# Optimization experiments

Measured on AMD Instinct MI355X. Metric: run time of the kernel, lower is better.

## Reference

```python
import jax, jax.numpy as jnp
import numpy as np
from jax import lax

STRIDES = (8, 16, 32)
FEAT_SIZES = ((80, 80), (40, 40), (20, 20))  # 640x640 input
NUM_CLASSES = 80
NMS_THR = 0.65
SCORE_THR = 0.01
NMS_PRE = 1000
MAX_PER_IMG = 100


def make_points():
    # MlvlPointGenerator.grid_priors with offset=0, with_stride=True.
    pts = []
    for (h, w), s in zip(FEAT_SIZES, STRIDES):
        y, x = jnp.meshgrid(jnp.arange(h, dtype=jnp.float32),
                            jnp.arange(w, dtype=jnp.float32), indexing='ij')
        pts.append(jnp.stack([x.ravel() * s, y.ravel() * s,
                              jnp.full(h * w, float(s)),
                              jnp.full(h * w, float(s))], axis=-1))
    return jnp.concatenate(pts, axis=0)  # [P, 4] = (px, py, sx, sy)


def decode_boxes(points, reg):
    # YOLOXBBoxDecoder: xy = reg[:2]*stride + point; wh = exp(reg[2:])*stride
    xys = reg[..., :2] * points[..., 2:] + points[..., :2]
    whs = jnp.exp(reg[..., 2:]) * points[..., 2:]
    half = whs * 0.5
    return jnp.concatenate([xys - half, xys + half], axis=-1)  # [..., 4] xyxy


def pairwise_iou(b):
    # b: [N, 4] xyxy
    area = (b[:, 2] - b[:, 0]) * (b[:, 3] - b[:, 1])
    lt = jnp.maximum(b[:, None, :2], b[None, :, :2])
    rb = jnp.minimum(b[:, None, 2:], b[None, :, 2:])
    wh = jnp.clip(rb - lt, 0.0)
    inter = wh[..., 0] * wh[..., 1]
    return inter / (area[:, None] + area[None, :] - inter + 1e-9)


def nms_image(cls_s, boxes, obj):
    # cls_s: [P, C] sigmoid scores, boxes: [P, 4], obj: [P] sigmoid objectness
    max_scores = jnp.max(cls_s, axis=-1)
    labels = jnp.argmax(cls_s, axis=-1)
    scores = max_scores * obj
    masked = jnp.where(scores >= SCORE_THR, scores, -1.0)
    top_scores, top_idx = lax.top_k(masked, NMS_PRE)  # sorted descending
    valid = top_scores >= SCORE_THR
    b = boxes[top_idx]            # [K, 4]
    lab = labels[top_idx]         # [K]
    # batched_nms: offset boxes per class so cross-class boxes never overlap
    off = lab.astype(b.dtype)[:, None] * (jnp.max(jnp.abs(b)) + 1.0)
    iou = pairwise_iou(b + off)   # [K, K]
    idx = jnp.arange(NMS_PRE)

    def body(i, keep):
        sup = (iou[i] > NMS_THR) & keep[i] & (idx > i)
        return keep & ~sup

    keep = lax.fori_loop(0, NMS_PRE, body, valid)
    # compact kept detections (score-sorted order preserved), pad to MAX_PER_IMG
    order = jnp.argsort(~keep, stable=True)[:MAX_PER_IMG]
    k = keep[order]
    out_b = jnp.where(k[:, None], b[order], 0.0)
    out_s = jnp.where(k, top_scores[order], 0.0)
    out_l = jnp.where(k, lab[order], -1)
    return out_b, out_s, out_l


def setup_inputs() -> dict:
    key = jax.random.key(0)
    ks = jax.random.split(key, 9)
    shapes = {
        'cls0': (32, NUM_CLASSES, 80, 80), 'cls1': (32, NUM_CLASSES, 40, 40),
        'cls2': (32, NUM_CLASSES, 20, 20),
        'reg0': (32, 4, 80, 80), 'reg1': (32, 4, 40, 40), 'reg2': (32, 4, 20, 20),
        'obj0': (32, 1, 80, 80), 'obj1': (32, 1, 40, 40), 'obj2': (32, 1, 20, 20),
    }
    return {n: jax.random.normal(k, s, dtype=jnp.float32)
            for (n, s), k in zip(shapes.items(), ks)}


def reference(cls0, cls1, cls2, reg0, reg1, reg2, obj0, obj1, obj2):
    def flat(xs, c):
        return jnp.concatenate(
            [jnp.transpose(x, (0, 2, 3, 1)).reshape(x.shape[0], -1, c) for x in xs],
            axis=1)
    cls = flat([cls0, cls1, cls2], NUM_CLASSES)   # [N, P, C]
    reg = flat([reg0, reg1, reg2], 4)             # [N, P, 4]
    obj = flat([obj0, obj1, obj2], 1)[..., 0]     # [N, P]
    points = make_points()                        # [P, 4]
    boxes = decode_boxes(points[None], reg)       # [N, P, 4]
    cls = jax.nn.sigmoid(cls)
    obj = jax.nn.sigmoid(obj)
    return jax.vmap(nms_image)(cls, boxes, obj)   # ([N,M,4],[N,M],[N,M] labels)
```

## Files before the change

### kernel.cpp

```cpp
#include <hip/hip_runtime.h>
#include <stdint.h>

#define N_IMG 32
#define P_TOT 8400
#define NCLS 80
#define NMS_PRE 1000
#define MAXOUT 100
#define SCORE_THRF 0.01f
#define NMS_THRF 0.65f
#define CAND_N 2048
#define NB 512
#define BINBASE 8192
#define TIE_EPS 0.05f


__device__ __forceinline__ float sigmoidf_(float x) { return 1.0f / (1.0f + expf(-x)); }

__global__ __launch_bounds__(256) void k_score(
    const float* __restrict__ cls0, const float* __restrict__ cls1, const float* __restrict__ cls2,
    const float* __restrict__ obj0, const float* __restrict__ obj1, const float* __restrict__ obj2,
    uint64_t* __restrict__ keys)
{
    __shared__ float    pml[4][64];
    __shared__ uint64_t part[4][64];
    int lane = threadIdx.x & 63, wid = threadIdx.x >> 6;
    int a = blockIdx.x * 64 + lane;
    int n = a / P_TOT;
    int p = a - n * P_TOT;

    const float* cl; const float* ob; int HW, q;
    if (p < 6400)      { cl = cls0; ob = obj0; HW = 6400; q = p; }
    else if (p < 8000) { cl = cls1; ob = obj1; HW = 1600; q = p - 6400; }
    else               { cl = cls2; ob = obj2; HW = 400;  q = p - 8000; }

    const float* cbase = cl + (size_t)n * NCLS * HW + q;
    int c0 = wid * 20;

    float lg[20];
    #pragma unroll
    for (int i = 0; i < 20; ++i)
        lg[i] = cbase[(size_t)(c0 + i) * HW];
    __builtin_amdgcn_sched_group_barrier(0x20, 20, 0);

    float a0 = fmaxf(lg[0], lg[1]),  a1 = fmaxf(lg[2], lg[3]);
    float a2 = fmaxf(lg[4], lg[5]),  a3 = fmaxf(lg[6], lg[7]);
    float a4 = fmaxf(lg[8], lg[9]),  a5 = fmaxf(lg[10], lg[11]);
    float a6 = fmaxf(lg[12], lg[13]), a7 = fmaxf(lg[14], lg[15]);
    float a8 = fmaxf(lg[16], lg[17]), a9 = fmaxf(lg[18], lg[19]);
    float b0 = fmaxf(a0, a1), b1 = fmaxf(a2, a3), b2 = fmaxf(a4, a5);
    float b3 = fmaxf(a6, a7), b4 = fmaxf(a8, a9);
    float lmax = fmaxf(fmaxf(fmaxf(b0, b1), fmaxf(b2, b3)), b4);
    pml[wid][lane] = lmax;
    __syncthreads();

    float gmaxl = fmaxf(fmaxf(pml[0][lane], pml[1][lane]),
                        fmaxf(pml[2][lane], pml[3][lane]));
    float thr = gmaxl - TIE_EPS;
    uint64_t m = 0;
    #pragma unroll
    for (int i = 0; i < 20; ++i) {
        if (lg[i] >= thr) {
            float s = sigmoidf_(lg[i]);
            uint64_t pk = ((uint64_t)__float_as_uint(s) << 8) | (uint32_t)(79 - (c0 + i));
            m = m > pk ? m : pk;
        }
    }
    part[wid][lane] = m;
    __syncthreads();

    if (wid == 0) {
        uint64_t m0 = part[0][lane], m1 = part[1][lane];
        uint64_t m2 = part[2][lane], m3 = part[3][lane];
        uint64_t ma = m0 > m1 ? m0 : m1, mb = m2 > m3 ? m2 : m3;
        uint64_t mm = ma > mb ? ma : mb;
        float best = __uint_as_float((uint32_t)(mm >> 8));
        int bc = 79 - (int)(mm & 0xFFu);

        float so = sigmoidf_(ob[(size_t)n * HW + q]);
        float sc = __fmul_rn(best, so);
        float masked = (sc >= SCORE_THRF) ? sc : -1.0f;
        uint32_t u = __float_as_uint(masked);
        uint32_t ord = (u & 0x80000000u) ? ~u : (u | 0x80000000u);
        uint32_t dk = ~ord;
        keys[a] = ((uint64_t)dk << 32) | (uint32_t)((p << 8) | bc);
    }
}

__global__ __launch_bounds__(1024) void k_selnms(
    const uint64_t* __restrict__ keys,
    const float* __restrict__ reg0, const float* __restrict__ reg1, const float* __restrict__ reg2,
    float* __restrict__ out)
{
    __shared__ __align__(16) char big[60416];
    __shared__ int   s_misc[2];
    __shared__ float fsh[17];
    __shared__ int   kidx[MAXOUT];

    uint64_t* cand    = (uint64_t*)big;
    uint32_t* hist    = (uint32_t*)(big + 16384);
    uint32_t* base    = (uint32_t*)(big + 18432);
    uint32_t* fill    = (uint32_t*)(big + 20480);
    uint64_t* grouped = (uint64_t*)(big + 22528);
    float4* s_obx = (float4*)(big + 16384);
    float*  s_oar = (float*) (big + 32384);
    float4* s_raw = (float4*)(big + 36384);
    float2* s_sl  = (float2*)(big + 52384);

    int n = blockIdx.x, tid = threadIdx.x;

    if (tid < NB) { hist[tid] = 0; fill[tid] = 0; }
    for (int t = tid; t < CAND_N; t += 1024) cand[t] = ~0ull;
    __syncthreads();

    #pragma unroll
    for (int it = 0; it < 9; ++it) {
        int t = tid + it * 1024;
        if (t < P_TOT) {
            uint64_t k = keys[(size_t)n * P_TOT + t];
            uint32_t dk = (uint32_t)(k >> 32);
            if (!(dk & 0x80000000u)) atomicAdd(&hist[(dk >> 17) - BINBASE], 1u);
        }
    }
    __syncthreads();

    if (tid < 64) {
        uint32_t c[8]; uint32_t s = 0;
        #pragma unroll
        for (int i = 0; i < 8; ++i) { c[i] = hist[tid * 8 + i]; s += c[i]; }
        uint32_t inc = s;
        #pragma unroll
        for (int o = 1; o < 64; o <<= 1) {
            uint32_t v = __shfl_up(inc, o);
            if (tid >= o) inc += v;
        }
        uint32_t excl = inc - s;
        uint32_t b = excl;
        #pragma unroll
        for (int i = 0; i < 8; ++i) { base[tid * 8 + i] = b; b += c[i]; }
        uint32_t total = __shfl(inc, 63);
        uint32_t target = total < (uint32_t)NMS_PRE ? total : (uint32_t)NMS_PRE;
        uint32_t cum = excl; int found = 0x7fffffff;
        #pragma unroll
        for (int i = 0; i < 8; ++i) {
            cum += c[i];
            if (found == 0x7fffffff && cum >= target && target > 0) found = tid * 8 + i;
        }
        #pragma unroll
        for (int o = 32; o > 0; o >>= 1) { int f = __shfl_xor(found, o); found = f < found ? f : found; }
        if (tid == 0) { s_misc[0] = (total > 0) ? found : -1; s_misc[1] = (int)target; }
    }
    __syncthreads();
    int Bcut = s_misc[0];

    #pragma unroll
    for (int it = 0; it < 9; ++it) {
        int t = tid + it * 1024;
        if (t < P_TOT) {
            uint64_t k = keys[(size_t)n * P_TOT + t];
            uint32_t dk = (uint32_t)(k >> 32);
            if (!(dk & 0x80000000u)) {
                int bin = (int)((dk >> 17) - BINBASE);
                if (bin <= Bcut) {
                    uint32_t pos = base[bin] + atomicAdd(&fill[bin], 1u);
                    if (pos < CAND_N) grouped[pos] = k;
                }
            }
        }
    }
    __syncthreads();

    int ccnt = 0;
    if (Bcut >= 0) {
        uint32_t cc = base[Bcut] + hist[Bcut];
        ccnt = cc < (uint32_t)CAND_N ? (int)cc : CAND_N;
    }
    for (int s = tid; s < ccnt; s += 1024) {
        uint64_t k = grouped[s];
        uint32_t dk = (uint32_t)(k >> 32);
        int bin = (int)((dk >> 17) - BINBASE);
        uint32_t b0 = base[bin];
        uint32_t e0 = b0 + hist[bin]; if (e0 > (uint32_t)CAND_N) e0 = CAND_N;
        uint32_t r = b0;
        for (uint32_t t = b0; t < e0; ++t) r += (grouped[t] < k) ? 1u : 0u;
        if (r < (uint32_t)CAND_N) cand[r] = k;
    }
    int V = s_misc[1];
    __syncthreads();

    float4 bx = make_float4(0.f, 0.f, 0.f, 0.f);
    float scm = -1.0f, labf = 0.f, m = 0.f;
    if (tid < NMS_PRE) {
        uint64_t key = cand[tid];
        uint32_t dk = (uint32_t)(key >> 32);
        if (!(dk & 0x80000000u)) {
            uint32_t low = (uint32_t)key;
            int lab = (int)(low & 0xFFu);
            int p   = (int)(low >> 8);
            uint32_t ord = ~dk;
            scm = __uint_as_float(ord ^ 0x80000000u);

            const float* rg; int HW, q, W; float s;
            if (p < 6400)      { rg = reg0; HW = 6400; q = p;        W = 80; s = 8.f; }
            else if (p < 8000) { rg = reg1; HW = 1600; q = p - 6400; W = 40; s = 16.f; }
            else               { rg = reg2; HW = 400;  q = p - 8000; W = 20; s = 32.f; }

            float px = (float)(q % W) * s;
            float py = (float)(q / W) * s;
            const float* rb = rg + (size_t)n * 4 * HW + q;
            float dx = rb[0], dy = rb[HW], dw = rb[2 * HW], dh = rb[3 * HW];
            float cx = __fadd_rn(__fmul_rn(dx, s), px);
            float cy = __fadd_rn(__fmul_rn(dy, s), py);
            float hw = __fmul_rn(__fmul_rn(expf(dw), s), 0.5f);
            float hh = __fmul_rn(__fmul_rn(expf(dh), s), 0.5f);
            bx.x = __fsub_rn(cx, hw); bx.y = __fsub_rn(cy, hh);
            bx.z = __fadd_rn(cx, hw); bx.w = __fadd_rn(cy, hh);
            labf = (float)lab;
            m = fmaxf(fmaxf(fabsf(bx.x), fabsf(bx.y)), fmaxf(fabsf(bx.z), fabsf(bx.w)));
        }
    }

    #pragma unroll
    for (int o = 32; o > 0; o >>= 1) m = fmaxf(m, __shfl_xor(m, o));
    if ((tid & 63) == 0) fsh[tid >> 6] = m;
    __syncthreads();
    if (tid == 0) {
        float g = fsh[0];
        #pragma unroll
        for (int w = 1; w < 16; ++w) g = fmaxf(g, fsh[w]);
        fsh[16] = g;
    }
    __syncthreads();
    float gmax = fsh[16];

    if (tid < NMS_PRE) {
        float off = __fmul_rn(labf, __fadd_rn(gmax, 1.0f));
        float x1 = __fadd_rn(bx.x, off), y1 = __fadd_rn(bx.y, off);
        float x2 = __fadd_rn(bx.z, off), y2 = __fadd_rn(bx.w, off);
        s_obx[tid] = make_float4(x1, y1, x2, y2);
        s_oar[tid] = __fmul_rn(__fsub_rn(x2, x1), __fsub_rn(y2, y1));
        s_raw[tid] = bx;
        s_sl[tid]  = make_float2(scm, labf);
    }
    __syncthreads();
    if (tid >= 64) return;

    int lane = tid;
    int count = 0;
    float k1x1 = 0.f, k1y1 = 0.f, k1x2 = 0.f, k1y2 = 0.f, k1a = 0.f;
    float k2x1 = 0.f, k2y1 = 0.f, k2x2 = 0.f, k2y2 = 0.f, k2a = 0.f;

    float4 nb = s_obx[0]; float na = s_oar[0];
    for (int i = 0; i < V && count < MAXOUT; ++i) {
        float4 cb = nb; float ca = na;
        int ip = (i + 1 < V) ? i + 1 : i;
        nb = s_obx[ip]; na = s_oar[ip];

        bool sup = false;
        int c1 = count < 64 ? count : 64;
        if (lane < c1) {
            float ltx = fmaxf(k1x1, cb.x), lty = fmaxf(k1y1, cb.y);
            float rbx = fminf(k1x2, cb.z), rby = fminf(k1y2, cb.w);
            float w = fmaxf(__fsub_rn(rbx, ltx), 0.f);
            float h = fmaxf(__fsub_rn(rby, lty), 0.f);
            float inter = __fmul_rn(w, h);
            float denom = __fadd_rn(__fsub_rn(__fadd_rn(k1a, ca), inter), 1e-9f);
            sup = (inter / denom > NMS_THRF);
        }
        if (count > 64 && lane < count - 64) {
            float ltx = fmaxf(k2x1, cb.x), lty = fmaxf(k2y1, cb.y);
            float rbx = fminf(k2x2, cb.z), rby = fminf(k2y2, cb.w);
            float w = fmaxf(__fsub_rn(rbx, ltx), 0.f);
            float h = fmaxf(__fsub_rn(rby, lty), 0.f);
            float inter = __fmul_rn(w, h);
            float denom = __fadd_rn(__fsub_rn(__fadd_rn(k2a, ca), inter), 1e-9f);
            sup = sup || (inter / denom > NMS_THRF);
        }
        if (__ballot(sup) == 0ull) {
            if (lane == count)      { k1x1 = cb.x; k1y1 = cb.y; k1x2 = cb.z; k1y2 = cb.w; k1a = ca; }
            if (lane + 64 == count) { k2x1 = cb.x; k2y1 = cb.y; k2x2 = cb.z; k2y2 = cb.w; k2a = ca; }
            if (lane == 0) kidx[count] = i;
            ++count;
        }
    }

    float* ob = out;
    float* os = out + N_IMG * MAXOUT * 4;
    float* ol = os + N_IMG * MAXOUT;
    for (int mi = lane; mi < MAXOUT; mi += 64) {
        int o4 = (n * MAXOUT + mi) * 4;
        if (mi < count) {
            int i = kidx[mi];
            float4 b  = s_raw[i];
            float2 sl = s_sl[i];
            ob[o4 + 0] = b.x; ob[o4 + 1] = b.y; ob[o4 + 2] = b.z; ob[o4 + 3] = b.w;
            os[n * MAXOUT + mi] = sl.x;
            ol[n * MAXOUT + mi] = sl.y;
        } else {
            ob[o4 + 0] = 0.f; ob[o4 + 1] = 0.f; ob[o4 + 2] = 0.f; ob[o4 + 3] = 0.f;
            os[n * MAXOUT + mi] = 0.f;
            ol[n * MAXOUT + mi] = -1.f;
        }
    }
}

extern "C" void kernel_launch(void* const* d_in, const int* in_sizes, int n_in,
                              void* d_out, int out_size, void* d_ws, size_t ws_size,
                              hipStream_t stream)
{
    const float* cls0 = (const float*)d_in[0];
    const float* cls1 = (const float*)d_in[1];
    const float* cls2 = (const float*)d_in[2];
    const float* reg0 = (const float*)d_in[3];
    const float* reg1 = (const float*)d_in[4];
    const float* reg2 = (const float*)d_in[5];
    const float* obj0 = (const float*)d_in[6];
    const float* obj1 = (const float*)d_in[7];
    const float* obj2 = (const float*)d_in[8];

    uint64_t* keys = (uint64_t*)d_ws;
    float* out = (float*)d_out;

    k_score<<<(N_IMG * P_TOT) / 64, 256, 0, stream>>>(
        cls0, cls1, cls2, obj0, obj1, obj2, keys);
    k_selnms<<<N_IMG, 1024, 0, stream>>>(keys, reg0, reg1, reg2, out);
}
```

Measured before the change: 67.85 us.

## Process all classes per thread in score kernel; cache bin ids in LDS

```diff
diff --git a/kernel.cpp b/kernel.cpp
--- a/kernel.cpp
+++ b/kernel.cpp
@@ -21,10 +21,8 @@
     const float* __restrict__ obj0, const float* __restrict__ obj1, const float* __restrict__ obj2,
     uint64_t* __restrict__ keys)
 {
-    __shared__ float    pml[4][64];
-    __shared__ uint64_t part[4][64];
-    int lane = threadIdx.x & 63, wid = threadIdx.x >> 6;
-    int a = blockIdx.x * 64 + lane;
+    int wid = threadIdx.x >> 6, lane = threadIdx.x & 63;
+    int a = (blockIdx.x * 4 + wid) * 64 + lane;
     int n = a / P_TOT;
     int p = a - n * P_TOT;
 
@@ -34,56 +32,51 @@
     else               { cl = cls2; ob = obj2; HW = 400;  q = p - 8000; }
 
     const float* cbase = cl + (size_t)n * NCLS * HW + q;
-    int c0 = wid * 20;
-
-    float lg[20];
-    #pragma unroll
-    for (int i = 0; i < 20; ++i)
-        lg[i] = cbase[(size_t)(c0 + i) * HW];
-    __builtin_amdgcn_sched_group_barrier(0x20, 20, 0);
-
-    float a0 = fmaxf(lg[0], lg[1]),  a1 = fmaxf(lg[2], lg[3]);
-    float a2 = fmaxf(lg[4], lg[5]),  a3 = fmaxf(lg[6], lg[7]);
-    float a4 = fmaxf(lg[8], lg[9]),  a5 = fmaxf(lg[10], lg[11]);
-    float a6 = fmaxf(lg[12], lg[13]), a7 = fmaxf(lg[14], lg[15]);
-    float a8 = fmaxf(lg[16], lg[17]), a9 = fmaxf(lg[18], lg[19]);
-    float b0 = fmaxf(a0, a1), b1 = fmaxf(a2, a3), b2 = fmaxf(a4, a5);
-    float b3 = fmaxf(a6, a7), b4 = fmaxf(a8, a9);
-    float lmax = fmaxf(fmaxf(fmaxf(b0, b1), fmaxf(b2, b3)), b4);
-    pml[wid][lane] = lmax;
-    __syncthreads();
-
-    float gmaxl = fmaxf(fmaxf(pml[0][lane], pml[1][lane]),
-                        fmaxf(pml[2][lane], pml[3][lane]));
+
+    float objv = ob[(size_t)n * HW + q];
+    float lg[NCLS];
+    #pragma unroll
+    for (int i = 0; i < NCLS; ++i)
+        lg[i] = cbase[(size_t)i * HW];
+    __builtin_amdgcn_sched_group_barrier(0x20, 81, 0);
+    #pragma unroll
+    for (int i = 0; i < NCLS; ++i)
+        asm volatile("" : "+v"(lg[i]));
+
+    float t40[40];
+    #pragma unroll
+    for (int i = 0; i < 40; ++i) t40[i] = fmaxf(lg[2 * i], lg[2 * i + 1]);
+    float t20[20];
+    #pragma unroll
+    for (int i = 0; i < 20; ++i) t20[i] = fmaxf(t40[2 * i], t40[2 * i + 1]);
+    float t10[10];
+    #pragma unroll
+    for (int i = 0; i < 10; ++i) t10[i] = fmaxf(t20[2 * i], t20[2 * i + 1]);
+    float t5[5];
+    #pragma unroll
+    for (int i = 0; i < 5; ++i) t5[i] = fmaxf(t10[2 * i], t10[2 * i + 1]);
+    float gmaxl = fmaxf(fmaxf(fmaxf(t5[0], t5[1]), fmaxf(t5[2], t5[3])), t5[4]);
+
     float thr = gmaxl - TIE_EPS;
     uint64_t m = 0;
     #pragma unroll
-    for (int i = 0; i < 20; ++i) {
+    for (int i = 0; i < NCLS; ++i) {
         if (lg[i] >= thr) {
             float s = sigmoidf_(lg[i]);
-            uint64_t pk = ((uint64_t)__float_as_uint(s) << 8) | (uint32_t)(79 - (c0 + i));
+            uint64_t pk = ((uint64_t)__float_as_uint(s) << 8) | (uint32_t)(79 - i);
             m = m > pk ? m : pk;
         }
     }
-    part[wid][lane] = m;
-    __syncthreads();
-
-    if (wid == 0) {
-        uint64_t m0 = part[0][lane], m1 = part[1][lane];
-        uint64_t m2 = part[2][lane], m3 = part[3][lane];
-        uint64_t ma = m0 > m1 ? m0 : m1, mb = m2 > m3 ? m2 : m3;
-        uint64_t mm = ma > mb ? ma : mb;
-        float best = __uint_as_float((uint32_t)(mm >> 8));
-        int bc = 79 - (int)(mm & 0xFFu);
-
-        float so = sigmoidf_(ob[(size_t)n * HW + q]);
-        float sc = __fmul_rn(best, so);
-        float masked = (sc >= SCORE_THRF) ? sc : -1.0f;
-        uint32_t u = __float_as_uint(masked);
-        uint32_t ord = (u & 0x80000000u) ? ~u : (u | 0x80000000u);
-        uint32_t dk = ~ord;
-        keys[a] = ((uint64_t)dk << 32) | (uint32_t)((p << 8) | bc);
-    }
+    float best = __uint_as_float((uint32_t)(m >> 8));
+    int bc = 79 - (int)(m & 0xFFu);
+
+    float so = sigmoidf_(objv);
+    float sc = __fmul_rn(best, so);
+    float masked = (sc >= SCORE_THRF) ? sc : -1.0f;
+    uint32_t u = __float_as_uint(masked);
+    uint32_t ord = (u & 0x80000000u) ? ~u : (u | 0x80000000u);
+    uint32_t dk = ~ord;
+    keys[a] = ((uint64_t)dk << 32) | (uint32_t)((p << 8) | bc);
 }
 
 __global__ __launch_bounds__(1024) void k_selnms(
@@ -91,22 +84,24 @@
     const float* __restrict__ reg0, const float* __restrict__ reg1, const float* __restrict__ reg2,
     float* __restrict__ out)
 {
-    __shared__ __align__(16) char big[60416];
+    __shared__ __align__(16) char big[55712];
     __shared__ int   s_misc[2];
     __shared__ float fsh[17];
     __shared__ int   kidx[MAXOUT];
 
-    uint64_t* cand    = (uint64_t*)big;
-    uint32_t* hist    = (uint32_t*)(big + 16384);
-    uint32_t* base    = (uint32_t*)(big + 18432);
-    uint32_t* fill    = (uint32_t*)(big + 20480);
-    uint64_t* grouped = (uint64_t*)(big + 22528);
-    float4* s_obx = (float4*)(big + 16384);
-    float*  s_oar = (float*) (big + 32384);
-    float4* s_raw = (float4*)(big + 36384);
-    float2* s_sl  = (float2*)(big + 52384);
+    uint16_t* bin16   = (uint16_t*)big;
+    uint32_t* hist    = (uint32_t*)(big + 16800);
+    uint32_t* base    = (uint32_t*)(big + 18848);
+    uint32_t* fill    = (uint32_t*)(big + 20896);
+    uint64_t* grouped = (uint64_t*)(big + 22944);
+    uint64_t* cand    = (uint64_t*)(big + 39328);
+    float4* s_obx = (float4*)big;
+    float*  s_oar = (float*) (big + 16000);
+    float4* s_raw = (float4*)(big + 20000);
+    float2* s_sl  = (float2*)(big + 36000);
 
     int n = blockIdx.x, tid = threadIdx.x;
+    const uint64_t* kbase = keys + (size_t)n * P_TOT;
 
     if (tid < NB) { hist[tid] = 0; fill[tid] = 0; }
     for (int t = tid; t < CAND_N; t += 1024) cand[t] = ~0ull;
@@ -116,9 +111,15 @@
     for (int it = 0; it < 9; ++it) {
         int t = tid + it * 1024;
         if (t < P_TOT) {
-            uint64_t k = keys[(size_t)n * P_TOT + t];
+            uint64_t k = kbase[t];
             uint32_t dk = (uint32_t)(k >> 32);
-            if (!(dk & 0x80000000u)) atomicAdd(&hist[(dk >> 17) - BINBASE], 1u);
+            uint16_t v = 0;
+            if (!(dk & 0x80000000u)) {
+                uint32_t bin = (dk >> 17) - BINBASE;
+                atomicAdd(&hist[bin], 1u);
+                v = (uint16_t)(bin + 1);
+            }
+            bin16[t] = v;
         }
     }
     __syncthreads();
@@ -156,13 +157,12 @@
     for (int it = 0; it < 9; ++it) {
         int t = tid + it * 1024;
         if (t < P_TOT) {
-            uint64_t k = keys[(size_t)n * P_TOT + t];
-            uint32_t dk = (uint32_t)(k >> 32);
-            if (!(dk & 0x80000000u)) {
-                int bin = (int)((dk >> 17) - BINBASE);
+            uint16_t v = bin16[t];
+            if (v != 0) {
+                int bin = (int)v - 1;
                 if (bin <= Bcut) {
                     uint32_t pos = base[bin] + atomicAdd(&fill[bin], 1u);
-                    if (pos < CAND_N) grouped[pos] = k;
+                    if (pos < CAND_N) grouped[pos] = kbase[t];
                 }
             }
         }
@@ -320,7 +320,7 @@
     uint64_t* keys = (uint64_t*)d_ws;
     float* out = (float*)d_out;
 
-    k_score<<<(N_IMG * P_TOT) / 64, 256, 0, stream>>>(
+    k_score<<<1050, 256, 0, stream>>>(
         cls0, cls1, cls2, obj0, obj1, obj2, keys);
     k_selnms<<<N_IMG, 1024, 0, stream>>>(keys, reg0, reg1, reg2, out);
 }
```

Measured after the change: 72.50 us. 1.07x slower.
